# Optimization experiments

Hardware: AMD Instinct MI355X
Metric: run time of the kernel (lower is better)

## Reference

```python
import jax, jax.numpy as jnp
import numpy as np

DIM = 512; D_STATE = 16; D_CONV = 4; EXPAND = 2; NSLICES = 5
NUMBER_GS = 3; LENGTH_GS = 2048
D_INNER = EXPAND * DIM
DT_RANK = (DIM + 15) // 16  # 32
B_SZ = 2; SEQ = 5120


def setup_inputs() -> dict:
    key = jax.random.key(0)
    ks = iter(jax.random.split(key, 48))
    def rn(shape, scale=0.02):
        return jax.random.normal(next(ks), shape, dtype=jnp.float32) * scale
    # S4D-real style A init, one per direction
    A_log = jnp.log(jnp.tile(jnp.arange(1, D_STATE + 1, dtype=jnp.float32)[None, :], (D_INNER, 1)))
    inp = {
        'x': jax.random.normal(next(ks), (B_SZ, SEQ, DIM), dtype=jnp.float32),
        'ln_g': jnp.ones((DIM,), jnp.float32), 'ln_b': jnp.zeros((DIM,), jnp.float32),
        'in_proj_w': rn((2 * D_INNER, DIM)),
        'out_proj_w': rn((DIM, D_INNER)),
        'lin_w': rn((1, DIM)), 'lin_b': jnp.zeros((1,), jnp.float32),
        'gse0': rn((LENGTH_GS,), 1.0), 'gse1': rn((LENGTH_GS,), 1.0), 'gse2': rn((LENGTH_GS,), 1.0),
    }
    for sfx in ('f', 'b', 's'):
        inp['conv_w_' + sfx] = rn((D_INNER, 1, D_CONV), 0.2)
        inp['conv_bias_' + sfx] = rn((D_INNER,), 0.2)
        inp['xproj_w_' + sfx] = rn((DT_RANK + 2 * D_STATE, D_INNER))
        inp['dt_w_' + sfx] = rn((D_INNER, DT_RANK), 0.1)
        inp['dt_bias_' + sfx] = rn((D_INNER,), 0.1) + jnp.log(jnp.expm1(jnp.float32(0.01)))
        inp['A_log_' + sfx] = A_log
        inp['D_' + sfx] = jnp.ones((D_INNER,), jnp.float32)
    return inp


def _lin_interp(v, s):
    # F.interpolate(mode='linear', align_corners=True) from len(v) to s
    L = v.shape[0]
    pos = jnp.arange(s, dtype=jnp.float32) * ((L - 1) / (s - 1))
    i0 = jnp.clip(jnp.floor(pos).astype(jnp.int32), 0, L - 2)
    w = pos - i0.astype(jnp.float32)
    return v[i0] * (1.0 - w) + v[i0 + 1] * w


def _branch(xz, conv_w, conv_bias, xproj_w, dt_w, dt_bias, A_log, Dp):
    # mamba_inner_fn_no_out_proj: xz (b, 2*d_inner, l) -> y (b, d_inner, l)
    x, z = jnp.split(xz, 2, axis=1)
    pad = conv_w.shape[-1] - 1
    xc = jax.lax.conv_general_dilated(
        jnp.pad(x, ((0, 0), (0, 0), (pad, 0))), conv_w, (1,), 'VALID',
        dimension_numbers=('NCH', 'OIH', 'NCH'), feature_group_count=x.shape[1])
    xc = jax.nn.silu(xc + conv_bias[None, :, None])
    x_dbl = jnp.einsum('bdl,kd->bkl', xc, xproj_w)  # (b, dt_rank+2n, l)
    dt, Bm, Cm = jnp.split(x_dbl, [DT_RANK, DT_RANK + D_STATE], axis=1)
    delta = jax.nn.softplus(jnp.einsum('brl,dr->bdl', dt, dt_w) + dt_bias[None, :, None])
    A = -jnp.exp(A_log)  # (d_inner, n)
    def step(h, inp):
        d_t, B_t, C_t, u_t = inp  # (b,d),(b,n),(b,n),(b,d)
        h = jnp.exp(d_t[..., None] * A) * h + d_t[..., None] * B_t[:, None, :] * u_t[..., None]
        return h, jnp.einsum('bdn,bn->bd', h, C_t)
    h0 = jnp.zeros((xc.shape[0], xc.shape[1], D_STATE), xc.dtype)
    scan_in = (jnp.moveaxis(delta, 2, 0), jnp.moveaxis(Bm, 2, 0),
               jnp.moveaxis(Cm, 2, 0), jnp.moveaxis(xc, 2, 0))
    _, ys = jax.lax.scan(step, h0, scan_in)  # (l, b, d)
    y = jnp.moveaxis(ys, 0, 2) + xc * Dp[None, :, None]
    return y * jax.nn.silu(z)


def reference(x, ln_g, ln_b, in_proj_w, out_proj_w, lin_w, lin_b, gse0, gse1, gse2,
              conv_w_f, conv_bias_f, xproj_w_f, dt_w_f, dt_bias_f, A_log_f, D_f,
              conv_w_b, conv_bias_b, xproj_w_b, dt_w_b, dt_bias_b, A_log_b, D_b,
              conv_w_s, conv_bias_s, xproj_w_s, dt_w_s, dt_bias_s, A_log_s, D_s):
    b, s, d = x.shape
    mu = jnp.mean(x, -1, keepdims=True)
    var = jnp.var(x, -1, keepdims=True)
    h = (x - mu) * jax.lax.rsqrt(var + 1e-5) * ln_g + ln_b
    h = jax.nn.relu(h)
    xz = jnp.einsum('bld,ed->bel', h, in_proj_w)  # (b, 2*d_inner, l)
    out_f = _branch(xz, conv_w_f, conv_bias_f, xproj_w_f, dt_w_f, dt_bias_f, A_log_f, D_f)
    out_b = jnp.flip(_branch(jnp.flip(xz, -1), conv_w_b, conv_bias_b, xproj_w_b, dt_w_b, dt_bias_b, A_log_b, D_b), -1)
    e = xz.shape[1]
    # xz.chunk(nslices, -1) -> stack(-1) -> flatten(-2)  == slice-interleave
    xz_s = jnp.swapaxes(xz.reshape(b, e, NSLICES, s // NSLICES), 2, 3).reshape(b, e, s)
    out_s = _branch(xz_s, conv_w_s, conv_bias_s, xproj_w_s, dt_w_s, dt_bias_s, A_log_s, D_s)
    out_s = jnp.swapaxes(out_s.reshape(b, D_INNER, NSLICES, s // NSLICES), 2, 3).reshape(b, D_INNER, s)
    y = jnp.einsum('bdl,od->blo', out_f + out_b + out_s, out_proj_w)  # (b, l, dim)
    individual_score = jax.nn.sigmoid(jnp.einsum('blo,ko->blk', y, lin_w) + lin_b)[:, :, 0]
    group_scores = jnp.stack([jax.nn.sigmoid(_lin_interp(g, s)) for g in (gse0, gse1, gse2)])
    return group_scores, individual_score
```

## Files before the change

kernel.cpp:

```cpp
#include <hip/hip_runtime.h>
#include <stdint.h>

#define SEQ  5120
#define DIMX 512
#define E2   2048
#define DI   1024
#define NST  16
#define DTR  32
#define KXP  64
#define LGS  2048
#define NSL  5
#define NSEG 8
#define SEGL 640

typedef unsigned short ushort_t;
typedef __attribute__((ext_vector_type(8))) __bf16 bf16x8;
typedef __attribute__((ext_vector_type(4))) float f32x4;

__device__ __forceinline__ float b2f(ushort_t u) {
  union { unsigned int i; float f; } v; v.i = ((unsigned int)u) << 16; return v.f;
}
__device__ __forceinline__ ushort_t f2b(float f) {
  union { float f; unsigned int i; } v; v.f = f;
  unsigned int u = v.i;
  return (ushort_t)((u + 0x7FFFu + ((u >> 16) & 1u)) >> 16);
}

#define AS1 __attribute__((address_space(1)))
#define AS3 __attribute__((address_space(3)))
__device__ __forceinline__ void glds16(const void* g, void* l) {
  __builtin_amdgcn_global_load_lds((const AS1 void*)g, (AS3 void*)l, 16, 0, 0);
}

__device__ __forceinline__ int pmap(int br, int t) {
  return (br == 0) ? t : (br == 1) ? (SEQ - 1 - t) : ((t % NSL) * 1024 + t / NSL);
}
__device__ __forceinline__ int omap(int br, int t) {
  return (br == 0) ? t : (br == 1) ? (SEQ - 1 - t) : ((t & 1023) * NSL + (t >> 10));
}

__device__ __forceinline__ float bfly16(const float* hC, int n) {
  float a8[8], a4[4], a2[2], y;
#pragma unroll
  for (int j = 0; j < 8; j++) {
    float keep = (n & 8) ? hC[j+8] : hC[j];
    float send = (n & 8) ? hC[j]   : hC[j+8];
    a8[j] = keep + __shfl_xor(send, 8, 64);
  }
#pragma unroll
  for (int j = 0; j < 4; j++) {
    float keep = (n & 4) ? a8[j+4] : a8[j];
    float send = (n & 4) ? a8[j]   : a8[j+4];
    a4[j] = keep + __shfl_xor(send, 4, 64);
  }
#pragma unroll
  for (int j = 0; j < 2; j++) {
    float keep = (n & 2) ? a4[j+2] : a4[j];
    float send = (n & 2) ? a4[j]   : a4[j+2];
    a2[j] = keep + __shfl_xor(send, 2, 64);
  }
  {
    float keep = (n & 1) ? a2[1] : a2[0];
    float send = (n & 1) ? a2[0] : a2[1];
    y = keep + __shfl_xor(send, 1, 64);
  }
  return y;
}

#define OFF_LWB   ((size_t)256)
#define OFF_LNGF  ((size_t)1280)
#define OFF_LNBF  ((size_t)3328)
#define OFF_LBF   ((size_t)5376)
#define OFF_CWF   ((size_t)5632)
#define OFF_CBF   ((size_t)54784)
#define OFF_DTBF  ((size_t)67072)
#define OFF_ALF   ((size_t)79360)
#define OFF_DDF   ((size_t)275968)
#define OFF_WEFF  ((size_t)288256)
#define OFF_SC    ((size_t)292352)
#define OFF_DTWB  ((size_t)333312)
#define OFF_XPWB  ((size_t)529920)
#define OFF_OPWB  ((size_t)923136)
#define OFF_INWB  ((size_t)1971712)
#define OFF_XD    ((size_t)4068864)
#define OFF_DLTB  ((size_t)8001024)
#define OFF_XZ    OFF_DLTB
#define OFF_BF    ((size_t)70915584)
#define OFF_CF    ((size_t)72881664)
#define OFF_HLOC  ((size_t)74847744)
#define OFF_HIN   ((size_t)77993472)
#define OFF_STOT  ((size_t)81139200)
#define OFF_UB    ((size_t)81335808)
#define OFF_H     OFF_UB
#define OFF_ZGB   ((size_t)144250368)

struct Ent { const void* s; void* d; int n; int fmt; };
struct Tab { Ent e[32]; };

__global__ __launch_bounds__(256) void k_import(Tab t, int cnt) {
  int id = blockIdx.y;
  if (id >= cnt) return;
  Ent E = t.e[id];
  int stride = gridDim.x * 256;
  const float* s = (const float*)E.s;
  if (E.fmt == 0) {
    ushort_t* dst = (ushort_t*)E.d;
    for (int i = blockIdx.x * 256 + threadIdx.x; i < E.n; i += stride) dst[i] = f2b(s[i]);
  } else {
    float* dst = (float*)E.d;
    for (int i = blockIdx.x * 256 + threadIdx.x; i < E.n; i += stride) dst[i] = s[i];
  }
}

__global__ __launch_bounds__(256) void k_ln(const float* __restrict__ x,
    const float* __restrict__ gam, const float* __restrict__ bet,
    ushort_t* __restrict__ h) {
  int token = blockIdx.x * 4 + (threadIdx.x >> 6);
  int lane = threadIdx.x & 63;
  const float* row = x + (size_t)token * DIMX + lane * 8;
  float4 a0 = *(const float4*)(row);
  float4 a1 = *(const float4*)(row + 4);
  float v[8] = {a0.x,a0.y,a0.z,a0.w,a1.x,a1.y,a1.z,a1.w};
  float s = 0.f, ss = 0.f;
#pragma unroll
  for (int i = 0; i < 8; i++) { s += v[i]; ss += v[i]*v[i]; }
#pragma unroll
  for (int m = 1; m < 64; m <<= 1) { s += __shfl_xor(s, m, 64); ss += __shfl_xor(ss, m, 64); }
  float mean = s * (1.f / DIMX);
  float rs = rsqrtf(ss * (1.f / DIMX) - mean * mean + 1e-5f);
  ushort_t o[8];
#pragma unroll
  for (int i = 0; i < 8; i++) {
    float y = (v[i] - mean) * rs * gam[lane*8+i] + bet[lane*8+i];
    o[i] = f2b(fmaxf(y, 0.f));
  }
  ushort_t* orow = h + (size_t)token * DIMX + lane * 8;
  *(ushort4*)(orow)     = make_ushort4(o[0],o[1],o[2],o[3]);
  *(ushort4*)(orow + 4) = make_ushort4(o[4],o[5],o[6],o[7]);
}

__global__ __launch_bounds__(256) void k_inproj(const ushort_t* __restrict__ hA,
    const ushort_t* __restrict__ Wb, ushort_t* __restrict__ xz) {
  __shared__ ushort_t As[128*32];
  __shared__ ushort_t Bs[128*32];
  const int tid = threadIdx.x;
  const int w = tid >> 6, lane = tid & 63;
  const int wr = w >> 1, wc = w & 1;
  const int m0 = blockIdx.x * 128, n0 = blockIdx.y * 128;
  const int lrow = lane & 15, lko = (lane >> 4) * 8;
  f32x4 acc[4][4];
#pragma unroll
  for (int i = 0; i < 4; i++)
#pragma unroll
    for (int j = 0; j < 4; j++) acc[i][j] = (f32x4){0.f,0.f,0.f,0.f};
  for (int k0 = 0; k0 < DIMX; k0 += 32) {
    __syncthreads();
#pragma unroll
    for (int r = 0; r < 2; r++) {
      int e = r * 256 + tid;
      int row = e >> 2, seg = e & 3;
      glds16(hA + (size_t)(m0 + row) * DIMX + k0 + seg * 8, &As[row*32 + seg*8]);
      glds16(Wb + (size_t)(n0 + row) * DIMX + k0 + seg * 8, &Bs[row*32 + seg*8]);
    }
    __syncthreads();
    bf16x8 aF[4], bF[4];
#pragma unroll
    for (int i = 0; i < 4; i++)
      aF[i] = *(const bf16x8*)&As[(wr*64 + i*16 + lrow)*32 + lko];
#pragma unroll
    for (int j = 0; j < 4; j++)
      bF[j] = *(const bf16x8*)&Bs[(wc*64 + j*16 + lrow)*32 + lko];
#pragma unroll
    for (int i = 0; i < 4; i++)
#pragma unroll
      for (int j = 0; j < 4; j++)
        acc[i][j] = __builtin_amdgcn_mfma_f32_16x16x32_bf16(aF[i], bF[j], acc[i][j], 0, 0, 0);
  }
#pragma unroll
  for (int i = 0; i < 4; i++)
#pragma unroll
    for (int j = 0; j < 4; j++)
#pragma unroll
      for (int r = 0; r < 4; r++) {
        int m = m0 + wr*64 + i*16 + (lane>>4)*4 + r;
        int n = n0 + wc*64 + j*16 + lrow;
        xz[(size_t)m * E2 + n] = f2b(acc[i][j][r]);
      }
}

__global__ __launch_bounds__(256) void k_conv(const ushort_t* __restrict__ xz,
    const float* __restrict__ cwA, const float* __restrict__ cbA,
    ushort_t* __restrict__ uB) {
  __shared__ ushort_t xs[67][64];
  int ch = blockIdx.z, br = ch >> 1, b = ch & 1;
  int t0 = blockIdx.x * 64, d0 = blockIdx.y * 64;
  int tid = threadIdx.x, col = tid & 63, rg = tid >> 6;
  const float* cw = cwA + (size_t)br * DI * 4;
  const float* cb = cbA + (size_t)br * DI;
#pragma unroll
  for (int i = 0; i < 17; i++) {
    int row = rg + i * 4;
    if (row < 67) {
      int tau = t0 - 3 + row;
      ushort_t val = 0;
      if (tau >= 0) val = xz[((size_t)b * SEQ + pmap(br, tau)) * E2 + d0 + col];
      xs[row][col] = val;
    }
  }
  __syncthreads();
  int d = d0 + col;
  float w0 = cw[d*4+0], w1 = cw[d*4+1], w2 = cw[d*4+2], w3 = cw[d*4+3];
  float bias = cb[d];
  size_t dbbase = ((size_t)(ch * 64 + (d >> 4))) * SEQ;
#pragma unroll
  for (int i = 0; i < 16; i++) {
    int ti = rg + i * 4;
    float a = bias + w0*b2f(xs[ti][col]) + w1*b2f(xs[ti+1][col])
                   + w2*b2f(xs[ti+2][col]) + w3*b2f(xs[ti+3][col]);
    float val = a / (1.f + __expf(-a));
    uB[(dbbase + t0 + ti) * 16 + (col & 15)] = f2b(val);
  }
}

__global__ __launch_bounds__(256) void k_zg(const ushort_t* __restrict__ xz,
    const float* __restrict__ weff, ushort_t* __restrict__ zgB) {
  int b = blockIdx.z;
  int l0 = blockIdx.x * 64, d0 = blockIdx.y * 64;
  int tid = threadIdx.x, col = tid & 63, rg = tid >> 6;
  int d = d0 + col;
  float wef = weff[d];
  size_t dbbase = ((size_t)(b * 64 + (d >> 4))) * SEQ;
#pragma unroll
  for (int i = 0; i < 16; i++) {
    int l = l0 + rg + i * 4;
    float zr = b2f(xz[((size_t)b * SEQ + l) * E2 + DI + d]);
    float z = zr / (1.f + __expf(-zr));
    zgB[(dbbase + l) * 16 + (col & 15)] = f2b(z * wef);
  }
}

__global__ __launch_bounds__(256) void k_xdbl(const ushort_t* __restrict__ uB,
    const ushort_t* __restrict__ xpwA, ushort_t* __restrict__ xdA) {
  __shared__ ushort_t As[64*32];
  __shared__ ushort_t Bs[64*32];
  int ch = blockIdx.y, br = ch >> 1;
  const ushort_t* xpw = xpwA + (size_t)br * KXP * DI;
  ushort_t* xd = xdA + (size_t)ch * SEQ * KXP;
  int t0 = blockIdx.x * 64;
  int tid = threadIdx.x, w = tid >> 6, lane = tid & 63;
  int lrow = lane & 15, lko = (lane >> 4) * 8;
  int row = tid >> 2, seg = tid & 3;
  f32x4 acc[4];
#pragma unroll
  for (int j = 0; j < 4; j++) acc[j] = (f32x4){0.f,0.f,0.f,0.f};
  for (int k0 = 0; k0 < DI; k0 += 32) {
    __syncthreads();
    glds16(uB + (((size_t)(ch*64 + (k0>>4) + (seg>>1)) * SEQ + t0 + row) * 16 + (seg&1)*8),
           &As[row*32 + seg*8]);
    glds16(xpw + (size_t)row * DI + k0 + seg * 8, &Bs[row*32 + seg*8]);
    __syncthreads();
    bf16x8 aF = *(const bf16x8*)&As[(w*16 + lrow)*32 + lko];
#pragma unroll
    for (int j = 0; j < 4; j++) {
      bf16x8 bF = *(const bf16x8*)&Bs[(j*16 + lrow)*32 + lko];
      acc[j] = __builtin_amdgcn_mfma_f32_16x16x32_bf16(aF, bF, acc[j], 0, 0, 0);
    }
  }
#pragma unroll
  for (int j = 0; j < 4; j++)
#pragma unroll
    for (int r = 0; r < 4; r++) {
      int t = t0 + w*16 + (lane>>4)*4 + r;
      xd[(size_t)t * KXP + j*16 + lrow] = f2b(acc[j][r]);
    }
}

__global__ __launch_bounds__(256) void k_bc(const ushort_t* __restrict__ xdA,
    float* __restrict__ Bf, float* __restrict__ Cf) {
  __shared__ float tb[128][34];
  int ch = blockIdx.y, t0 = blockIdx.x * 128;
  int tid = threadIdx.x;
  const ushort_t* xdb = xdA + (size_t)ch * SEQ * KXP;
#pragma unroll
  for (int i = 0; i < 2; i++) {
    int r = (tid >> 2) + i * 64;
    int q = tid & 3;
    const ushort_t* p = xdb + (size_t)(t0 + r) * KXP + 32 + q * 8;
    uint4 v = *(const uint4*)p;
    unsigned int wd[4] = {v.x, v.y, v.z, v.w};
    float* dst = &tb[r][q * 8];
#pragma unroll
    for (int j = 0; j < 4; j++) {
      dst[2*j]   = __uint_as_float(wd[j] << 16);
      dst[2*j+1] = __uint_as_float(wd[j] & 0xFFFF0000u);
    }
  }
  __syncthreads();
  int nn = tid >> 4, sg = tid & 15;
  float ob[8], oc[8];
#pragma unroll
  for (int j = 0; j < 8; j++) {
    ob[j] = tb[sg*8 + j][nn];
    oc[j] = tb[sg*8 + j][16 + nn];
  }
  float* Bp = Bf + ((size_t)ch * NST + nn) * SEQ + t0 + sg * 8;
  float* Cp = Cf + ((size_t)ch * NST + nn) * SEQ + t0 + sg * 8;
  *(float4*)Bp       = make_float4(ob[0],ob[1],ob[2],ob[3]);
  *(float4*)(Bp + 4) = make_float4(ob[4],ob[5],ob[6],ob[7]);
  *(float4*)Cp       = make_float4(oc[0],oc[1],oc[2],oc[3]);
  *(float4*)(Cp + 4) = make_float4(oc[4],oc[5],oc[6],oc[7]);
}

__global__ __launch_bounds__(256) void k_delta(const ushort_t* __restrict__ xdA,
    const ushort_t* __restrict__ dtwb, const float* __restrict__ dtbf,
    ushort_t* __restrict__ dltB) {
  __shared__ ushort_t As[128*32];
  __shared__ ushort_t Bs[128*32];
  int ch = blockIdx.z, br = ch >> 1;
  int t0 = blockIdx.x * 128, d0 = blockIdx.y * 128;
  int tid = threadIdx.x, w = tid >> 6, lane = tid & 63;
  int wr = w >> 1, wc = w & 1;
  int lrow = lane & 15, lko = (lane >> 4) * 8;
  const ushort_t* xdb = xdA + (size_t)ch * SEQ * KXP;
  const ushort_t* dwp = dtwb + (size_t)br * DI * DTR;
#pragma unroll
  for (int r = 0; r < 2; r++) {
    int e = r * 256 + tid;
    int row = e >> 2, seg = e & 3;
    glds16(xdb + (size_t)(t0 + row) * KXP + seg * 8, &As[row*32 + seg*8]);
    glds16(dwp + (size_t)(d0 + row) * DTR + seg * 8, &Bs[row*32 + seg*8]);
  }
  __syncthreads();
  bf16x8 aF[4], bF[4];
#pragma unroll
  for (int i = 0; i < 4; i++)
    aF[i] = *(const bf16x8*)&As[(wr*64 + i*16 + lrow)*32 + lko];
#pragma unroll
  for (int j = 0; j < 4; j++)
    bF[j] = *(const bf16x8*)&Bs[(wc*64 + j*16 + lrow)*32 + lko];
  f32x4 acc[4][4];
#pragma unroll
  for (int i = 0; i < 4; i++)
#pragma unroll
    for (int j = 0; j < 4; j++) {
      acc[i][j] = (f32x4){0.f,0.f,0.f,0.f};
      acc[i][j] = __builtin_amdgcn_mfma_f32_16x16x32_bf16(aF[i], bF[j], acc[i][j], 0, 0, 0);
    }
#pragma unroll
  for (int i = 0; i < 4; i++)
#pragma unroll
    for (int j = 0; j < 4; j++)
#pragma unroll
      for (int r = 0; r < 4; r++) {
        int t = t0 + wr*64 + i*16 + (lane>>4)*4 + r;
        int d = d0 + wc*64 + j*16 + lrow;
        float xv = acc[i][j][r] + dtbf[br * DI + d];
        float sp = (xv > 20.f) ? xv : log1pf(__expf(xv));
        dltB[(((size_t)(ch*64 + (d>>4))) * SEQ + t) * 16 + (d & 15)] = f2b(sp);
      }
}

__global__ __launch_bounds__(128, 5) void k_scan1(
    const ushort_t* __restrict__ dltB, const ushort_t* __restrict__ uB,
    const ushort_t* __restrict__ zgB, const float* __restrict__ Bf,
    const float* __restrict__ Cf, const float* __restrict__ alf,
    const float* __restrict__ ddf, float* __restrict__ sc,
    float* __restrict__ Hloc, float* __restrict__ Stot) {
  __shared__ __align__(16) float BS[2][16][18];
  __shared__ __align__(16) float CS[2][16][18];
  __shared__ __align__(16) float4 dd4[2][4][17];
  __shared__ float2 gS[2][4][17];
  int bid = blockIdx.x;
  int dblk = bid & 63, seg = (bid >> 6) & 7, ch = bid >> 9;
  int br = ch >> 1, b = ch & 1;
  int tid = threadIdx.x, w = tid >> 6, lane = tid & 63, g = lane >> 4, n = lane & 15;
  int da = w * 8 + g;
  int db = da + 4;
  int dA = dblk * 16 + da, dB = dblk * 16 + db;
  const float L2E = 1.4426950408889634f;
  float ApA = -__expf(alf[br * (DI*NST) + dA * NST + n]) * L2E;
  float ApB = -__expf(alf[br * (DI*NST) + dB * NST + n]) * L2E;
  float DdA = ddf[br * DI + dA], DdB = ddf[br * DI + dB];
  const ushort_t* dlp = dltB + ((size_t)(ch * 64 + dblk) * SEQ) * 16;
  const ushort_t* uBp = uB   + ((size_t)(ch * 64 + dblk) * SEQ) * 16;
  const ushort_t* zgp = zgB  + ((size_t)(b  * 64 + dblk) * SEQ) * 16;
  const float* Bfp = Bf + ((size_t)ch * NST) * SEQ;
  const float* Cfp = Cf + ((size_t)ch * NST) * SEQ;
  float* srow = sc + (size_t)b * SEQ;
  float hstA = 0.f, hstB = 0.f, SaccA = 0.f, SaccB = 0.f;
  int sn = lane >> 2, sq = lane & 3;
  for (int t0 = seg * SEGL; t0 < seg * SEGL + SEGL; t0 += 16) {
    *(float4*)&BS[w][sn][sq*4] = *(const float4*)&Bfp[(size_t)sn * SEQ + t0 + sq*4];
    *(float4*)&CS[w][sn][sq*4] = *(const float4*)&Cfp[(size_t)sn * SEQ + t0 + sq*4];
    size_t rowo = (size_t)(t0 + n) * 16;
    float dltA = b2f(dlp[rowo + da]);
    float dltBv = b2f(dlp[rowo + db]);
    float uA = b2f(uBp[rowo + da]);
    float uBv = b2f(uBp[rowo + db]);
    size_t growo = (size_t)pmap(br, t0 + n) * 16;
    float gA = b2f(zgp[growo + da]);
    float gB = b2f(zgp[growo + db]);
    SaccA += dltA; SaccB += dltBv;
    dd4[w][g][n] = make_float4(dltA, dltA * uA, dltBv, dltBv * uBv);
    gS[w][g][n]  = make_float2(gA, gB);
    float dug = fmaf(DdA * uA, gA, DdB * uBv * gB);
    float Bk[16], Ck[16];
#pragma unroll
    for (int j = 0; j < 4; j++) {
      *(float4*)&Bk[j*4] = *(const float4*)&BS[w][n][j*4];
      *(float4*)&Ck[j*4] = *(const float4*)&CS[w][n][j*4];
    }
    float hC[16];
#pragma unroll
    for (int k = 0; k < 16; k++) {
      float4 v = dd4[w][g][k];
      float2 gg = gS[w][g][k];
      hstA = fmaf(__builtin_amdgcn_exp2f(v.x * ApA), hstA, v.y * Bk[k]);
      hstB = fmaf(__builtin_amdgcn_exp2f(v.z * ApB), hstB, v.w * Bk[k]);
      hC[k] = fmaf(hstA, gg.x, hstB * gg.y) * Ck[k];
    }
    float y = bfly16(hC, n) + dug;
    y += __shfl_xor(y, 16, 64);
    y += __shfl_xor(y, 32, 64);
    if (lane < 16) atomicAdd(srow + omap(br, t0 + lane), y);
  }
  Hloc[(((size_t)ch * NSEG + seg) * 1024 + dA) * 16 + n] = hstA;
  Hloc[(((size_t)ch * NSEG + seg) * 1024 + dB) * 16 + n] = hstB;
#pragma unroll
  for (int m = 1; m < 16; m <<= 1) {
    SaccA += __shfl_xor(SaccA, m, 64);
    SaccB += __shfl_xor(SaccB, m, 64);
  }
  if (n == 0) {
    Stot[((size_t)ch * NSEG + seg) * 1024 + dA] = SaccA;
    Stot[((size_t)ch * NSEG + seg) * 1024 + dB] = SaccB;
  }
}

__global__ __launch_bounds__(256) void k_stitch(const float* __restrict__ Stot,
    const float* __restrict__ Hloc, const float* __restrict__ alf,
    float* __restrict__ Hin) {
  int idx = blockIdx.x * 256 + threadIdx.x;
  int ch = idx >> 14, rem = idx & 16383, d = rem >> 4, n = rem & 15;
  int br = ch >> 1;
  float A = -__expf(alf[(size_t)br * (DI*NST) + d * NST + n]);
  float h = 0.f;
  for (int s = 0; s < NSEG; s++) {
    size_t base = ((size_t)ch * NSEG + s) * 1024 + d;
    Hin[base * 16 + n] = h;
    h = __expf(A * Stot[base]) * h + Hloc[base * 16 + n];
  }
}

__global__ __launch_bounds__(256, 2) void k_scan2(
    const ushort_t* __restrict__ zgB, const ushort_t* __restrict__ dltB,
    const float* __restrict__ Cf, const float* __restrict__ alf,
    const float* __restrict__ Hin, float* __restrict__ sc) {
  __shared__ float red[4][72];
  int ch = blockIdx.x >> 6, grp = blockIdx.x & 63;
  int seg = blockIdx.y + 1;
  int br = ch >> 1, b = ch & 1;
  int tid = threadIdx.x, w = tid >> 6, lane = tid & 63;
  int dsub4 = w * 4;
  int dbase = grp * 16 + dsub4;
  const float L2E = 1.4426950408889634f;
  float A2[4][16], Hn[4][16];
#pragma unroll
  for (int q = 0; q < 4; q++) {
    int d = dbase + q;
#pragma unroll
    for (int nn = 0; nn < 16; nn++)
      A2[q][nn] = -__expf(alf[(size_t)br * (DI*NST) + d * NST + nn]) * L2E;
    const float* hp = Hin + (((size_t)ch * NSEG + seg) * 1024 + d) * 16;
#pragma unroll
    for (int nn = 0; nn < 16; nn++) Hn[q][nn] = hp[nn];
  }
  const ushort_t* dlp = dltB + ((size_t)(ch * 64 + grp) * SEQ) * 16;
  const ushort_t* zgp = zgB  + ((size_t)(b  * 64 + grp) * SEQ) * 16;
  const float* Cfp = Cf + (size_t)ch * NST * SEQ;
  float* srow = sc + (size_t)b * SEQ;
  float c0 = 0.f, c1 = 0.f, c2 = 0.f, c3 = 0.f;
  for (int w0 = seg * SEGL; w0 < seg * SEGL + SEGL; w0 += 64) {
    int t = w0 + lane;
    uint2 dv = *(const uint2*)(dlp + (size_t)t * 16 + dsub4);
    float S0 = b2f((ushort_t)(dv.x & 0xFFFF));
    float S1 = b2f((ushort_t)(dv.x >> 16));
    float S2 = b2f((ushort_t)(dv.y & 0xFFFF));
    float S3 = b2f((ushort_t)(dv.y >> 16));
#pragma unroll
    for (int ofs = 1; ofs < 64; ofs <<= 1) {
      float v0 = __shfl_up(S0, ofs, 64);
      float v1 = __shfl_up(S1, ofs, 64);
      float v2 = __shfl_up(S2, ofs, 64);
      float v3 = __shfl_up(S3, ofs, 64);
      if (lane >= ofs) { S0 += v0; S1 += v1; S2 += v2; S3 += v3; }
    }
    float t0_ = __shfl(S0, 63, 64), t1_ = __shfl(S1, 63, 64);
    float t2_ = __shfl(S2, 63, 64), t3_ = __shfl(S3, 63, 64);
    S0 += c0; c0 += t0_;
    S1 += c1; c1 += t1_;
    S2 += c2; c2 += t2_;
    S3 += c3; c3 += t3_;
    float r0 = 0.f, r1 = 0.f, r2 = 0.f, r3 = 0.f;
#pragma unroll
    for (int nn = 0; nn < 16; nn++) {
      float Cn = Cfp[(size_t)nn * SEQ + t];
      r0 = fmaf(Cn * Hn[0][nn], __builtin_amdgcn_exp2f(A2[0][nn] * S0), r0);
      r1 = fmaf(Cn * Hn[1][nn], __builtin_amdgcn_exp2f(A2[1][nn] * S1), r1);
      r2 = fmaf(Cn * Hn[2][nn], __builtin_amdgcn_exp2f(A2[2][nn] * S2), r2);
      r3 = fmaf(Cn * Hn[3][nn], __builtin_amdgcn_exp2f(A2[3][nn] * S3), r3);
    }
    uint2 zv = *(const uint2*)(zgp + (size_t)pmap(br, t) * 16 + dsub4);
    float g0 = b2f((ushort_t)(zv.x & 0xFFFF));
    float g1 = b2f((ushort_t)(zv.x >> 16));
    float g2 = b2f((ushort_t)(zv.y & 0xFFFF));
    float g3 = b2f((ushort_t)(zv.y >> 16));
    float y = fmaf(r0, g0, fmaf(r1, g1, fmaf(r2, g2, r3 * g3)));
    red[w][lane] = y;
    __syncthreads();
    if (w == 0) {
      float ytot = red[0][lane] + red[1][lane] + red[2][lane] + red[3][lane];
      atomicAdd(srow + omap(br, t), ytot);
    }
    __syncthreads();
  }
}

__global__ __launch_bounds__(256) void k_weff_init(const ushort_t* __restrict__ opwb,
    const ushort_t* __restrict__ lwb, float* __restrict__ weff, float* __restrict__ sc) {
  int i = blockIdx.x * 256 + threadIdx.x;
  if (i < DI) {
    float s = 0.f;
    for (int o = 0; o < DIMX; o++) s += b2f(lwb[o]) * b2f(opwb[(size_t)o * DI + i]);
    weff[i] = s;
  }
  int j = i - DI;
  if (j >= 0 && j < 2 * SEQ) sc[j] = 0.f;
}

__global__ __launch_bounds__(256) void k_out(const float* __restrict__ g0,
    const float* __restrict__ g1, const float* __restrict__ g2,
    const float* __restrict__ sc, const float* __restrict__ lbf,
    float* __restrict__ out) {
  int idx = blockIdx.x * 256 + threadIdx.x;
  if (idx < 3 * SEQ) {
    int j = idx / SEQ, t = idx % SEQ;
    const float* g = (j == 0) ? g0 : (j == 1) ? g1 : g2;
    float pos = t * ((float)(LGS - 1) / (float)(SEQ - 1));
    int i0 = (int)floorf(pos);
    if (i0 < 0) i0 = 0; if (i0 > LGS - 2) i0 = LGS - 2;
    float wt = pos - (float)i0;
    float v = g[i0] * (1.f - wt) + g[i0 + 1] * wt;
    out[idx] = 1.f / (1.f + __expf(-v));
  } else if (idx < 5 * SEQ) {
    float t = sc[idx - 3 * SEQ] + lbf[0];
    out[idx] = 1.f / (1.f + __expf(-t));
  }
}

extern "C" void kernel_launch(void* const* d_in, const int* in_sizes, int n_in,
                              void* d_out, int out_size, void* d_ws, size_t ws_size,
                              hipStream_t stream) {
  char* ws = (char*)d_ws;
  ushort_t* lwb   = (ushort_t*)(ws + OFF_LWB);
  float*    lngf  = (float*)(ws + OFF_LNGF);
  float*    lnbf  = (float*)(ws + OFF_LNBF);
  float*    lbf   = (float*)(ws + OFF_LBF);
  float*    cwf   = (float*)(ws + OFF_CWF);
  float*    cbf   = (float*)(ws + OFF_CBF);
  float*    dtbf  = (float*)(ws + OFF_DTBF);
  float*    alf   = (float*)(ws + OFF_ALF);
  float*    ddf   = (float*)(ws + OFF_DDF);
  float*    weff  = (float*)(ws + OFF_WEFF);
  float*    sc    = (float*)(ws + OFF_SC);
  ushort_t* dtwb  = (ushort_t*)(ws + OFF_DTWB);
  ushort_t* xpwb  = (ushort_t*)(ws + OFF_XPWB);
  ushort_t* opwb  = (ushort_t*)(ws + OFF_OPWB);
  ushort_t* inwb  = (ushort_t*)(ws + OFF_INWB);
  ushort_t* xd    = (ushort_t*)(ws + OFF_XD);
  ushort_t* dltB  = (ushort_t*)(ws + OFF_DLTB);
  ushort_t* xz    = (ushort_t*)(ws + OFF_XZ);
  float*    Bf    = (float*)(ws + OFF_BF);
  float*    Cf    = (float*)(ws + OFF_CF);
  ushort_t* uB    = (ushort_t*)(ws + OFF_UB);
  ushort_t* h     = (ushort_t*)(ws + OFF_H);
  ushort_t* zgB   = (ushort_t*)(ws + OFF_ZGB);
  float*    Hloc  = (float*)(ws + OFF_HLOC);
  float*    Hin   = (float*)(ws + OFF_HIN);
  float*    Stot  = (float*)(ws + OFF_STOT);
  float*    OUT   = (float*)d_out;

  Tab tab;
  int c = 0;
  tab.e[c++] = {d_in[3], inwb, E2 * DIMX, 0};
  tab.e[c++] = {d_in[4], opwb, DIMX * DI, 0};
  tab.e[c++] = {d_in[5], lwb, DIMX, 0};
  for (int br = 0; br < 3; br++) {
    int base = 10 + br * 7;
    tab.e[c++] = {d_in[base + 2], xpwb + (size_t)br * KXP * DI, KXP * DI, 0};
    tab.e[c++] = {d_in[base + 3], dtwb + (size_t)br * DI * DTR, DI * DTR, 0};
  }
  tab.e[c++] = {d_in[1], lngf, DIMX, 1};
  tab.e[c++] = {d_in[2], lnbf, DIMX, 1};
  tab.e[c++] = {d_in[6], lbf, 1, 1};
  for (int br = 0; br < 3; br++) {
    int base = 10 + br * 7;
    tab.e[c++] = {d_in[base + 0], cwf + (size_t)br * DI * 4, DI * 4, 1};
    tab.e[c++] = {d_in[base + 1], cbf + (size_t)br * DI, DI, 1};
    tab.e[c++] = {d_in[base + 4], dtbf + (size_t)br * DI, DI, 1};
    tab.e[c++] = {d_in[base + 5], alf + (size_t)br * DI * NST, DI * NST, 1};
    tab.e[c++] = {d_in[base + 6], ddf + (size_t)br * DI, DI, 1};
  }

  dim3 blk(256);
  k_import<<<dim3(64, c), blk, 0, stream>>>(tab, c);
  k_weff_init<<<44, blk, 0, stream>>>(opwb, lwb, weff, sc);
  k_ln<<<2560, blk, 0, stream>>>((const float*)d_in[0], lngf, lnbf, h);
  k_inproj<<<dim3(80, 16), blk, 0, stream>>>(h, inwb, xz);
  k_conv<<<dim3(80, 16, 6), blk, 0, stream>>>(xz, cwf, cbf, uB);
  k_zg<<<dim3(80, 16, 2), blk, 0, stream>>>(xz, weff, zgB);
  k_xdbl<<<dim3(80, 6), blk, 0, stream>>>(uB, xpwb, xd);
  k_bc<<<dim3(40, 6), blk, 0, stream>>>(xd, Bf, Cf);
  k_delta<<<dim3(40, 8, 6), blk, 0, stream>>>(xd, dtwb, dtbf, dltB);
  k_scan1<<<3072, dim3(128), 0, stream>>>(dltB, uB, zgB, Bf, Cf, alf, ddf,
                                          sc, Hloc, Stot);
  k_stitch<<<384, blk, 0, stream>>>(Stot, Hloc, alf, Hin);
  k_scan2<<<dim3(384, NSEG - 1), blk, 0, stream>>>(zgB, dltB, Cf, alf, Hin, sc);
  k_out<<<100, blk, 0, stream>>>((const float*)d_in[7], (const float*)d_in[8],
                                 (const float*)d_in[9], sc, lbf, OUT);
}
```

Before: 680.1 us.

## Process four channels per thread in scan1 with vectorized bf16 loads

Each thread in the first-pass selective scan now carries four inner channels instead of two. That halves the block count and amortizes each B/C shared-memory tile and each atomicAdd over twice as many channels. The per-timestep delta, u and gate values are loaded as packed 4×bf16 (uint2) vectors instead of scalar shorts. The cost is more registers per thread (launch bounds lowered to 4 waves), fewer blocks for latency hiding, and a longer serial dependency chain per step.

```diff
diff --git a/kernel.cpp b/kernel.cpp
--- a/kernel.cpp
+++ b/kernel.cpp
@@ -360,7 +360,7 @@
       }
 }
 
-__global__ __launch_bounds__(128, 5) void k_scan1(
+__global__ __launch_bounds__(128, 4) void k_scan1(
     const ushort_t* __restrict__ dltB, const ushort_t* __restrict__ uB,
     const ushort_t* __restrict__ zgB, const float* __restrict__ Bf,
     const float* __restrict__ Cf, const float* __restrict__ alf,
@@ -368,42 +368,50 @@
     float* __restrict__ Hloc, float* __restrict__ Stot) {
   __shared__ __align__(16) float BS[2][16][18];
   __shared__ __align__(16) float CS[2][16][18];
-  __shared__ __align__(16) float4 dd4[2][4][17];
-  __shared__ float2 gS[2][4][17];
+  __shared__ __align__(16) float4 ddl[2][4][17];
+  __shared__ __align__(16) float4 ddu[2][4][17];
+  __shared__ __align__(16) float4 gS4[2][4][17];
   int bid = blockIdx.x;
-  int dblk = bid & 63, seg = (bid >> 6) & 7, ch = bid >> 9;
+  int dblk = bid & 31, seg = (bid >> 5) & 7, ch = bid >> 8;
   int br = ch >> 1, b = ch & 1;
   int tid = threadIdx.x, w = tid >> 6, lane = tid & 63, g = lane >> 4, n = lane & 15;
-  int da = w * 8 + g;
-  int db = da + 4;
-  int dA = dblk * 16 + da, dB = dblk * 16 + db;
+  int rb = dblk * 2 + w;
+  int dqb = rb * 16 + g * 4;
   const float L2E = 1.4426950408889634f;
-  float ApA = -__expf(alf[br * (DI*NST) + dA * NST + n]) * L2E;
-  float ApB = -__expf(alf[br * (DI*NST) + dB * NST + n]) * L2E;
-  float DdA = ddf[br * DI + dA], DdB = ddf[br * DI + dB];
-  const ushort_t* dlp = dltB + ((size_t)(ch * 64 + dblk) * SEQ) * 16;
-  const ushort_t* uBp = uB   + ((size_t)(ch * 64 + dblk) * SEQ) * 16;
-  const ushort_t* zgp = zgB  + ((size_t)(b  * 64 + dblk) * SEQ) * 16;
+  float Ap[4], Dd[4];
+#pragma unroll
+  for (int q = 0; q < 4; q++) {
+    Ap[q] = -__expf(alf[br * (DI*NST) + (dqb + q) * NST + n]) * L2E;
+    Dd[q] = ddf[br * DI + dqb + q];
+  }
+  const ushort_t* dlp = dltB + ((size_t)(ch * 64 + rb) * SEQ) * 16;
+  const ushort_t* uBp = uB   + ((size_t)(ch * 64 + rb) * SEQ) * 16;
+  const ushort_t* zgp = zgB  + ((size_t)(b  * 64 + rb) * SEQ) * 16;
   const float* Bfp = Bf + ((size_t)ch * NST) * SEQ;
   const float* Cfp = Cf + ((size_t)ch * NST) * SEQ;
   float* srow = sc + (size_t)b * SEQ;
-  float hstA = 0.f, hstB = 0.f, SaccA = 0.f, SaccB = 0.f;
+  float hst[4] = {0.f, 0.f, 0.f, 0.f};
+  float Sacc[4] = {0.f, 0.f, 0.f, 0.f};
   int sn = lane >> 2, sq = lane & 3;
   for (int t0 = seg * SEGL; t0 < seg * SEGL + SEGL; t0 += 16) {
     *(float4*)&BS[w][sn][sq*4] = *(const float4*)&Bfp[(size_t)sn * SEQ + t0 + sq*4];
     *(float4*)&CS[w][sn][sq*4] = *(const float4*)&Cfp[(size_t)sn * SEQ + t0 + sq*4];
-    size_t rowo = (size_t)(t0 + n) * 16;
-    float dltA = b2f(dlp[rowo + da]);
-    float dltBv = b2f(dlp[rowo + db]);
-    float uA = b2f(uBp[rowo + da]);
-    float uBv = b2f(uBp[rowo + db]);
-    size_t growo = (size_t)pmap(br, t0 + n) * 16;
-    float gA = b2f(zgp[growo + da]);
-    float gB = b2f(zgp[growo + db]);
-    SaccA += dltA; SaccB += dltBv;
-    dd4[w][g][n] = make_float4(dltA, dltA * uA, dltBv, dltBv * uBv);
-    gS[w][g][n]  = make_float2(gA, gB);
-    float dug = fmaf(DdA * uA, gA, DdB * uBv * gB);
+    size_t rowo = (size_t)(t0 + n) * 16 + g * 4;
+    uint2 dv = *(const uint2*)(dlp + rowo);
+    uint2 uv = *(const uint2*)(uBp + rowo);
+    uint2 zv = *(const uint2*)(zgp + (size_t)pmap(br, t0 + n) * 16 + g * 4);
+    float dl0 = b2f((ushort_t)(dv.x & 0xFFFF)), dl1 = b2f((ushort_t)(dv.x >> 16));
+    float dl2 = b2f((ushort_t)(dv.y & 0xFFFF)), dl3 = b2f((ushort_t)(dv.y >> 16));
+    float u0 = b2f((ushort_t)(uv.x & 0xFFFF)), u1 = b2f((ushort_t)(uv.x >> 16));
+    float u2 = b2f((ushort_t)(uv.y & 0xFFFF)), u3 = b2f((ushort_t)(uv.y >> 16));
+    float gz0 = b2f((ushort_t)(zv.x & 0xFFFF)), gz1 = b2f((ushort_t)(zv.x >> 16));
+    float gz2 = b2f((ushort_t)(zv.y & 0xFFFF)), gz3 = b2f((ushort_t)(zv.y >> 16));
+    Sacc[0] += dl0; Sacc[1] += dl1; Sacc[2] += dl2; Sacc[3] += dl3;
+    ddl[w][g][n] = make_float4(dl0, dl1, dl2, dl3);
+    ddu[w][g][n] = make_float4(dl0*u0, dl1*u1, dl2*u2, dl3*u3);
+    gS4[w][g][n] = make_float4(gz0, gz1, gz2, gz3);
+    float dug = fmaf(Dd[0]*u0, gz0, fmaf(Dd[1]*u1, gz1,
+                fmaf(Dd[2]*u2, gz2, Dd[3]*u3*gz3)));
     float Bk[16], Ck[16];
 #pragma unroll
     for (int j = 0; j < 4; j++) {
@@ -413,27 +421,35 @@
     float hC[16];
 #pragma unroll
     for (int k = 0; k < 16; k++) {
-      float4 v = dd4[w][g][k];
-      float2 gg = gS[w][g][k];
-      hstA = fmaf(__builtin_amdgcn_exp2f(v.x * ApA), hstA, v.y * Bk[k]);
-      hstB = fmaf(__builtin_amdgcn_exp2f(v.z * ApB), hstB, v.w * Bk[k]);
-      hC[k] = fmaf(hstA, gg.x, hstB * gg.y) * Ck[k];
+      float4 L = ddl[w][g][k];
+      float4 U = ddu[w][g][k];
+      float4 G = gS4[w][g][k];
+      hst[0] = fmaf(__builtin_amdgcn_exp2f(L.x * Ap[0]), hst[0], U.x * Bk[k]);
+      hst[1] = fmaf(__builtin_amdgcn_exp2f(L.y * Ap[1]), hst[1], U.y * Bk[k]);
+      hst[2] = fmaf(__builtin_amdgcn_exp2f(L.z * Ap[2]), hst[2], U.z * Bk[k]);
+      hst[3] = fmaf(__builtin_amdgcn_exp2f(L.w * Ap[3]), hst[3], U.w * Bk[k]);
+      hC[k] = fmaf(hst[0], G.x, fmaf(hst[1], G.y,
+               fmaf(hst[2], G.z, hst[3] * G.w))) * Ck[k];
     }
     float y = bfly16(hC, n) + dug;
     y += __shfl_xor(y, 16, 64);
     y += __shfl_xor(y, 32, 64);
     if (lane < 16) atomicAdd(srow + omap(br, t0 + lane), y);
   }
-  Hloc[(((size_t)ch * NSEG + seg) * 1024 + dA) * 16 + n] = hstA;
-  Hloc[(((size_t)ch * NSEG + seg) * 1024 + dB) * 16 + n] = hstB;
+#pragma unroll
+  for (int q = 0; q < 4; q++)
+    Hloc[(((size_t)ch * NSEG + seg) * 1024 + dqb + q) * 16 + n] = hst[q];
 #pragma unroll
   for (int m = 1; m < 16; m <<= 1) {
-    SaccA += __shfl_xor(SaccA, m, 64);
-    SaccB += __shfl_xor(SaccB, m, 64);
+    Sacc[0] += __shfl_xor(Sacc[0], m, 64);
+    Sacc[1] += __shfl_xor(Sacc[1], m, 64);
+    Sacc[2] += __shfl_xor(Sacc[2], m, 64);
+    Sacc[3] += __shfl_xor(Sacc[3], m, 64);
   }
   if (n == 0) {
-    Stot[((size_t)ch * NSEG + seg) * 1024 + dA] = SaccA;
-    Stot[((size_t)ch * NSEG + seg) * 1024 + dB] = SaccB;
+#pragma unroll
+    for (int q = 0; q < 4; q++)
+      Stot[((size_t)ch * NSEG + seg) * 1024 + dqb + q] = Sacc[q];
   }
 }
 
@@ -622,7 +638,7 @@
   k_xdbl<<<dim3(80, 6), blk, 0, stream>>>(uB, xpwb, xd);
   k_bc<<<dim3(40, 6), blk, 0, stream>>>(xd, Bf, Cf);
   k_delta<<<dim3(40, 8, 6), blk, 0, stream>>>(xd, dtwb, dtbf, dltB);
-  k_scan1<<<3072, dim3(128), 0, stream>>>(dltB, uB, zgB, Bf, Cf, alf, ddf,
+  k_scan1<<<1536, dim3(128), 0, stream>>>(dltB, uB, zgB, Bf, Cf, alf, ddf,
                                           sc, Hloc, Stot);
   k_stitch<<<384, blk, 0, stream>>>(Stot, Hloc, alf, Hin);
   k_scan2<<<dim3(384, NSEG - 1), blk, 0, stream>>>(zgB, dltB, Cf, alf, Hin, sc);
```

New measurement: 647.6 us, median of 2. -4.8%, faster.
